# Kernel tuning notes

Measured on AMD Instinct MI355X. Metric: run time of the kernel, lower is better.

## Reference

```python
import jax, jax.numpy as jnp
import numpy as np

FILTER_P = 0.5
LOG_CLAMP = -100.0  # torch BCELoss clamps log terms at -100


def _zs_substep(img, step):
    """One Zhang-Suen thinning sub-iteration. img: int32 [H, W] in {0,1}.
    skimage.morphology.skeletonize uses Zhang-Suen for 2D inputs."""
    p = jnp.pad(img, 1)
    P2 = p[:-2, 1:-1]; P3 = p[:-2, 2:];  P4 = p[1:-1, 2:];  P5 = p[2:, 2:]
    P6 = p[2:, 1:-1];  P7 = p[2:, :-2];  P8 = p[1:-1, :-2]; P9 = p[:-2, :-2]
    nbrs = jnp.stack([P2, P3, P4, P5, P6, P7, P8, P9, P2])  # cyclic order
    B = nbrs[:8].sum(0)                                      # neighbor count
    A = ((nbrs[:-1] == 0) & (nbrs[1:] == 1)).sum(0)          # 0->1 transitions
    if step == 0:
        c1 = P2 * P4 * P6 == 0
        c2 = P4 * P6 * P8 == 0
    else:
        c1 = P2 * P4 * P8 == 0
        c2 = P2 * P6 * P8 == 0
    remove = (img == 1) & (B >= 2) & (B <= 6) & (A == 1) & c1 & c2
    return img * (1 - remove.astype(img.dtype))


def skeletonize(mask):
    """Zhang-Suen skeletonization. mask: bool [H, W] -> bool [H, W]."""
    img0 = mask.astype(jnp.int32)

    def body(state):
        img, _ = state
        new = _zs_substep(_zs_substep(img, 0), 1)
        return new, jnp.any(new != img)

    img, _ = jax.lax.while_loop(lambda s: s[1], body, (img0, jnp.bool_(True)))
    return img == 1


def setup_inputs() -> dict:
    key = jax.random.key(0)
    k1, k2 = jax.random.split(key)
    B, C, H, W = 8, 1, 512, 512
    pred = jax.random.uniform(k1, (B, C, H, W), dtype=jnp.float32)
    target = jax.random.uniform(k2, (B, C, H, W), dtype=jnp.float32)
    return {"pred": pred, "target": target}


def reference(pred, target):
    # [B, 1, H, W] -> [B, H, W]  (matches pred[i].squeeze(0))
    p2 = pred[:, 0]
    t2 = target[:, 0].astype(pred.dtype)

    gt_bin = t2 > 0.5
    pr_bin = p2 > FILTER_P
    gt_sk = jax.vmap(skeletonize)(gt_bin)
    pr_sk = jax.vmap(skeletonize)(pr_bin)

    # xor(and(gt_sk, pred_bin), gt_sk) == gt_sk & ~pred_bin (and symmetrically)
    positive_sel = gt_sk & (~pr_bin)
    negative_sel = pr_sk & (~gt_bin)
    sel = jax.lax.stop_gradient(positive_sel | negative_sel)

    # BCE with torch-style log clamping, masked mean per sample
    logp = jnp.clip(jnp.log(p2), LOG_CLAMP)
    log1mp = jnp.clip(jnp.log1p(-p2), LOG_CLAMP)
    bce = -(t2 * logp + (1.0 - t2) * log1mp)

    m = sel.astype(pred.dtype)
    cnt = m.sum(axis=(1, 2))                     # [B]
    per = jnp.where(cnt > 0,
                    (bce * m).sum(axis=(1, 2)) / jnp.maximum(cnt, 1.0),
                    0.0)
    total = per.sum() / pred.shape[0]
    return jnp.reshape(total, (1,))
```

## Files before the change

### kernel.cpp

```cpp
#include <hip/hip_runtime.h>
#include <stdint.h>

#define HW 512
#define WPR 8
#define IMG_WORDS (HW * WPR)
#define NIMG 8
#define PIX_PER_IMG (HW * HW)
#define TOTAL_PIX (NIMG * PIX_PER_IMG)
#define MASK_WORDS (TOTAL_PIX / 64)

#define NTASK 16
#define NSTRIP 16
#define SROWS 32
#define GW 16
#define BROWS 64
#define RSTRIDE 9
#define CS 16
#define MAXCHUNK 38

#define CONV_U32 (NTASK * 64)
#define HALO_U64 (NTASK * 15 * 2 * 2 * 128)

#define NBCE (TOTAL_PIX / 2048)

__global__ __launch_bounds__(256) void init_kernel(uint32_t* __restrict__ conv) {
#pragma unroll
    for (int k = 0; k < 4; ++k) conv[threadIdx.x + k * 256] = 0u;
}

__device__ __forceinline__ uint64_t zs1(int step, const uint64_t (&Uw)[3],
                                        const uint64_t (&Cw)[3],
                                        const uint64_t (&Dw)[3],
                                        uint64_t& NEW) {
    uint64_t P2 = Uw[1];
    uint64_t P6 = Dw[1];
    uint64_t P4 = (Cw[1] >> 1) | (Cw[2] << 63);
    uint64_t P8 = (Cw[1] << 1) | (Cw[0] >> 63);
    uint64_t P3 = (Uw[1] >> 1) | (Uw[2] << 63);
    uint64_t P9 = (Uw[1] << 1) | (Uw[0] >> 63);
    uint64_t P5 = (Dw[1] >> 1) | (Dw[2] << 63);
    uint64_t P7 = (Dw[1] << 1) | (Dw[0] >> 63);

    uint64_t s1 = P2 ^ P3, sum1 = s1 ^ P4, car1 = (P2 & P3) | (P4 & s1);
    uint64_t s2 = P5 ^ P6, sum2 = s2 ^ P7, car2 = (P5 & P6) | (P7 & s2);
    uint64_t s3 = sum1 ^ sum2, sum3 = s3 ^ P8, car3 = (sum1 & sum2) | (P8 & s3);
    uint64_t b0 = sum3 ^ P9, car4 = sum3 & P9;
    uint64_t s5 = car1 ^ car2, sum5 = s5 ^ car3, car5 = (car1 & car2) | (car3 & s5);
    uint64_t b1 = sum5 ^ car4, car6 = sum5 & car4;
    uint64_t b2 = car5 ^ car6, b3 = car5 & car6;
    uint64_t ge2 = b1 | b2 | b3;
    uint64_t le6 = ~(b3 | (b0 & b1 & b2));
    uint64_t condB = ge2 & le6;

    uint64_t t0 = ~P2 & P3, t1 = ~P3 & P4, t2 = ~P4 & P5, t3 = ~P5 & P6;
    uint64_t t4 = ~P6 & P7, t5 = ~P7 & P8, t6 = ~P8 & P9, t7 = ~P9 & P2;
    uint64_t a01 = t0 | t1, a23 = t2 | t3, a45 = t4 | t5, a67 = t6 | t7;
    uint64_t m2 = (t0 & t1) | (t2 & t3) | (t4 & t5) | (t6 & t7);
    uint64_t a0123 = a01 | a23, a4567 = a45 | a67;
    m2 |= (a01 & a23) | (a45 & a67);
    m2 |= a0123 & a4567;
    uint64_t condA = (a0123 | a4567) & ~m2;

    uint64_t c1, c2;
    if (step == 0) {
        uint64_t q = P4 & P6;
        c1 = ~(q & P2);
        c2 = ~(q & P8);
    } else {
        uint64_t q = P2 & P8;
        c1 = ~(q & P4);
        c2 = ~(q & P6);
    }
    uint64_t rem = Cw[1] & condB & condA & c1 & c2;
    NEW = Cw[1] & ~rem;
    return rem;
}

__global__ __launch_bounds__(512) void skel_kernel(const float* __restrict__ pred,
                                                   const float* __restrict__ target,
                                                   uint64_t* __restrict__ sk,
                                                   uint64_t* __restrict__ halo,
                                                   uint32_t* __restrict__ conv) {
    __shared__ uint64_t sbuf[2][BROWS * RSTRIDE];
    __shared__ int s_any8[8];
    __shared__ int s_dec;
    const int tid = threadIdx.x;
    const int task = blockIdx.x & (NTASK - 1);
    const int strip = blockIdx.x >> 4;
    const int rl = tid >> 3;
    const int wq = tid & 7;
    const int lane = tid & 63;
    const int wave = tid >> 6;
    const int gr0 = strip * SROWS - GW;
    const float* srcf = (task < 8 ? target : pred) + (size_t)(task & 7) * PIX_PER_IMG;
    uint64_t* dst = sk + (size_t)task * IMG_WORDS;

    for (int m = 0; m < 64; ++m) {
        int k = wave * 64 + m;
        int r = k >> 3, w = k & 7;
        int gr = gr0 + r;
        float f = (gr >= 0 && gr < HW) ? srcf[gr * HW + w * 64 + lane] : 0.0f;
        uint64_t bits = __ballot(f > 0.5f);
        if (lane == 0) sbuf[0][r * RSTRIDE + w] = bits;
    }
    __syncthreads();
    uint64_t C = sbuf[0][rl * RSTRIDE + wq];

    int cb = 0;
    const bool owned = (rl >= GW) && (rl < GW + SROWS);
    for (int chunk = 0; chunk < MAXCHUNK; ++chunk) {
        uint32_t tailch = 0;
        for (int ss = 0; ss < CS; ++ss) {
            const uint64_t* cur = sbuf[cb];
            uint64_t* nxt = sbuf[cb ^ 1];
            uint64_t Uw[3], Cw[3], Dw[3], NEW;
#pragma unroll
            for (int j = 0; j < 3; ++j) {
                int gw = wq - 1 + j;
                bool v = (gw >= 0) && (gw < 8);
                Uw[j] = (v && rl > 0)          ? cur[(rl - 1) * RSTRIDE + gw] : 0ull;
                Dw[j] = (v && rl < BROWS - 1)  ? cur[(rl + 1) * RSTRIDE + gw] : 0ull;
            }
            Cw[0] = (wq > 0) ? cur[rl * RSTRIDE + wq - 1] : 0ull;
            Cw[2] = (wq < 7) ? cur[rl * RSTRIDE + wq + 1] : 0ull;
            Cw[1] = C;
            uint64_t ch = zs1(ss & 1, Uw, Cw, Dw, NEW);
            if (ss >= CS - 2 && owned && ch) tailch = 1;
            nxt[rl * RSTRIDE + wq] = NEW;
            C = NEW;
            cb ^= 1;
            __syncthreads();
        }

        const int par = chunk & 1;
        if (strip > 0 && rl >= GW && rl < 2 * GW) {
            uint64_t* hp = halo + ((((size_t)task * 15 + (strip - 1)) * 2 + 0) * 2 + par) * 128
                                + (rl - GW) * 8 + wq;
            __hip_atomic_store(hp, C, __ATOMIC_RELAXED, __HIP_MEMORY_SCOPE_AGENT);
            asm volatile("s_waitcnt vmcnt(0)" ::: "memory");
        }
        if (strip < NSTRIP - 1 && rl >= 32 && rl < 48) {
            uint64_t* hp = halo + ((((size_t)task * 15 + strip) * 2 + 1) * 2 + par) * 128
                                + (rl - 32) * 8 + wq;
            __hip_atomic_store(hp, C, __ATOMIC_RELAXED, __HIP_MEMORY_SCOPE_AGENT);
            asm volatile("s_waitcnt vmcnt(0)" ::: "memory");
        }
        int wa = __any((int)tailch);
        if (lane == 0) s_any8[wave] = wa;
        __syncthreads();
        if (tid == 0) {
            int any = s_any8[0] | s_any8[1] | s_any8[2] | s_any8[3]
                    | s_any8[4] | s_any8[5] | s_any8[6] | s_any8[7];
            uint32_t add = 256u + (any ? 1u : 0u);
            uint32_t* cp = &conv[task * 64 + chunk];
            uint32_t v = __hip_atomic_fetch_add(cp, add, __ATOMIC_RELEASE,
                                                __HIP_MEMORY_SCOPE_AGENT) + add;
            while ((v >> 8) < (uint32_t)NSTRIP)
                v = __hip_atomic_load(cp, __ATOMIC_ACQUIRE, __HIP_MEMORY_SCOPE_AGENT);
            s_dec = ((v & 0xffu) != 0u) ? 1 : 0;
        }
        __syncthreads();
        if (!s_dec) break;

        if (strip > 0 && rl < GW) {
            const uint64_t* hp = halo + ((((size_t)task * 15 + (strip - 1)) * 2 + 1) * 2 + par) * 128
                                      + rl * 8 + wq;
            C = __hip_atomic_load(hp, __ATOMIC_RELAXED, __HIP_MEMORY_SCOPE_AGENT);
            sbuf[cb][rl * RSTRIDE + wq] = C;
        }
        if (strip < NSTRIP - 1 && rl >= 48) {
            const uint64_t* hp = halo + ((((size_t)task * 15 + strip) * 2 + 0) * 2 + par) * 128
                                      + (rl - 48) * 8 + wq;
            C = __hip_atomic_load(hp, __ATOMIC_RELAXED, __HIP_MEMORY_SCOPE_AGENT);
            sbuf[cb][rl * RSTRIDE + wq] = C;
        }
        __syncthreads();
    }

    if (owned) {
        int gr = gr0 + rl;
        dst[gr * WPR + wq] = C;
    }
}

__global__ __launch_bounds__(256) void bce_kernel(
        const float4* __restrict__ pred4, const float4* __restrict__ tgt4,
        const uint64_t* __restrict__ gt_sk, const uint64_t* __restrict__ pr_sk,
        float* __restrict__ psum, int* __restrict__ pcnt) {
    int tg = blockIdx.x * 256 + threadIdx.x;
    int w = tg >> 3;
    int sh = (tg & 7) * 8;
    uint32_t gbits = (uint32_t)(gt_sk[w] >> sh) & 0xffu;
    uint32_t pbits = (uint32_t)(pr_sk[w] >> sh) & 0xffu;
    float4 pa = pred4[2 * tg], pb = pred4[2 * tg + 1];
    float4 ta = tgt4[2 * tg], tb = tgt4[2 * tg + 1];
    float p[8] = {pa.x, pa.y, pa.z, pa.w, pb.x, pb.y, pb.z, pb.w};
    float t[8] = {ta.x, ta.y, ta.z, ta.w, tb.x, tb.y, tb.z, tb.w};
    float lsum = 0.0f;
    int lcnt = 0;
#pragma unroll
    for (int j = 0; j < 8; ++j) {
        float lp = fmaxf(logf(p[j]), -100.0f);
        float l1 = fmaxf(log1pf(-p[j]), -100.0f);
        float b = -(t[j] * lp + (1.0f - t[j]) * l1);
        uint32_t prb = (p[j] > 0.5f) ? 1u : 0u;
        uint32_t gtb = (t[j] > 0.5f) ? 1u : 0u;
        uint32_t m = (((gbits >> j) & 1u) & (prb ^ 1u))
                   | (((pbits >> j) & 1u) & (gtb ^ 1u));
        lsum = fmaf((float)m, b, lsum);
        lcnt += (int)m;
    }
#pragma unroll
    for (int off = 32; off > 0; off >>= 1) {
        lsum += __shfl_down(lsum, off, 64);
        lcnt += __shfl_down(lcnt, off, 64);
    }
    __shared__ float sred[4];
    __shared__ int cred[4];
    int wave = threadIdx.x >> 6, lane = threadIdx.x & 63;
    if (lane == 0) { sred[wave] = lsum; cred[wave] = lcnt; }
    __syncthreads();
    if (threadIdx.x == 0) {
        psum[blockIdx.x] = sred[0] + sred[1] + sred[2] + sred[3];
        pcnt[blockIdx.x] = cred[0] + cred[1] + cred[2] + cred[3];
    }
}

__global__ __launch_bounds__(1024) void final_kernel(const float* __restrict__ psum,
                                                     const int* __restrict__ pcnt,
                                                     float* __restrict__ out) {
    int t = threadIdx.x;
    float s = psum[t];
    int c = pcnt[t];
#pragma unroll
    for (int off = 32; off > 0; off >>= 1) {
        s += __shfl_down(s, off, 64);
        c += __shfl_down(c, off, 64);
    }
    __shared__ float ss[16];
    __shared__ int sc[16];
    int w = t >> 6;
    if ((t & 63) == 0) { ss[w] = s; sc[w] = c; }
    __syncthreads();
    if (t == 0) {
        float tot = 0.0f;
#pragma unroll
        for (int i = 0; i < NIMG; ++i) {
            float sv = ss[2 * i] + ss[2 * i + 1];
            int cv = sc[2 * i] + sc[2 * i + 1];
            tot += (cv > 0) ? sv / (float)cv : 0.0f;
        }
        out[0] = tot * (1.0f / NIMG);
    }
}

extern "C" void kernel_launch(void* const* d_in, const int* in_sizes, int n_in,
                              void* d_out, int out_size, void* d_ws, size_t ws_size,
                              hipStream_t stream) {
    const float* pred = (const float*)d_in[0];
    const float* target = (const float*)d_in[1];
    uint64_t* ws = (uint64_t*)d_ws;
    uint64_t* sk    = ws;
    uint64_t* gt_sk = sk;
    uint64_t* pr_sk = sk + MASK_WORDS;
    uint64_t* halo  = ws + 2 * MASK_WORDS;
    uint32_t* conv  = (uint32_t*)(halo + HALO_U64);
    float* psum     = (float*)(conv + CONV_U32);
    int* pcnt       = (int*)(psum + NBCE);

    init_kernel<<<1, 256, 0, stream>>>(conv);
    skel_kernel<<<NTASK * NSTRIP, 512, 0, stream>>>(pred, target, sk, halo, conv);
    bce_kernel<<<NBCE, 256, 0, stream>>>((const float4*)pred, (const float4*)target,
                                         gt_sk, pr_sk, psum, pcnt);
    final_kernel<<<1, 1024, 0, stream>>>(psum, pcnt, (float*)d_out);
}
```

Measured before the change: 111.0 us.

## Pre-pack binary masks in separate kernel and transpose skeleton LDS layout

Adds a pack_kernel that thresholds pred and target into bit masks across many blocks, and folds the convergence-counter zeroing into that kernel. The skeleton kernel now loads pre-packed 64-bit words instead of reading floats and running ballots per strip, including the redundant halo rows. Shared memory is transposed to word-column-major with stride 65, so each wave owns one word column across 64 rows. This shortens the serial prologue of the persistent skeleton blocks, at the cost of an extra launch and a global bitmask round trip.

```diff
diff --git a/kernel.cpp b/kernel.cpp
--- a/kernel.cpp
+++ b/kernel.cpp
@@ -14,7 +14,7 @@
 #define SROWS 32
 #define GW 16
 #define BROWS 64
-#define RSTRIDE 9
+#define LSTRIDE 65
 #define CS 16
 #define MAXCHUNK 38
 
@@ -23,9 +23,25 @@
 
 #define NBCE (TOTAL_PIX / 2048)
 
-__global__ __launch_bounds__(256) void init_kernel(uint32_t* __restrict__ conv) {
-#pragma unroll
-    for (int k = 0; k < 4; ++k) conv[threadIdx.x + k * 256] = 0u;
+__global__ void pack_kernel(const float* __restrict__ pred,
+                            const float* __restrict__ target,
+                            uint64_t* __restrict__ gt_bin,
+                            uint64_t* __restrict__ pr_bin,
+                            uint32_t* __restrict__ conv) {
+    int idx = blockIdx.x * 256 + threadIdx.x;
+    if (blockIdx.x < 4) {
+        int z = blockIdx.x * 256 + threadIdx.x;
+        conv[z] = 0u;
+    }
+    float p = pred[idx];
+    float t = target[idx];
+    uint64_t bp = __ballot(p > 0.5f);
+    uint64_t bt = __ballot(t > 0.5f);
+    if ((threadIdx.x & 63) == 0) {
+        int w = idx >> 6;
+        pr_bin[w] = bp;
+        gt_bin[w] = bt;
+    }
 }
 
 __device__ __forceinline__ uint64_t zs1(int step, const uint64_t (&Uw)[3],
@@ -76,35 +92,30 @@
     return rem;
 }
 
-__global__ __launch_bounds__(512) void skel_kernel(const float* __restrict__ pred,
-                                                   const float* __restrict__ target,
+__global__ __launch_bounds__(512) void skel_kernel(const uint64_t* __restrict__ bin,
                                                    uint64_t* __restrict__ sk,
                                                    uint64_t* __restrict__ halo,
                                                    uint32_t* __restrict__ conv) {
-    __shared__ uint64_t sbuf[2][BROWS * RSTRIDE];
+    __shared__ uint64_t sbuf[2][WPR * LSTRIDE];
     __shared__ int s_any8[8];
     __shared__ int s_dec;
     const int tid = threadIdx.x;
     const int task = blockIdx.x & (NTASK - 1);
     const int strip = blockIdx.x >> 4;
-    const int rl = tid >> 3;
-    const int wq = tid & 7;
-    const int lane = tid & 63;
-    const int wave = tid >> 6;
+    const int wq = tid >> 6;
+    const int rl = tid & 63;
     const int gr0 = strip * SROWS - GW;
-    const float* srcf = (task < 8 ? target : pred) + (size_t)(task & 7) * PIX_PER_IMG;
+    const uint64_t* src = bin + (size_t)task * IMG_WORDS;
     uint64_t* dst = sk + (size_t)task * IMG_WORDS;
 
-    for (int m = 0; m < 64; ++m) {
-        int k = wave * 64 + m;
-        int r = k >> 3, w = k & 7;
-        int gr = gr0 + r;
-        float f = (gr >= 0 && gr < HW) ? srcf[gr * HW + w * 64 + lane] : 0.0f;
-        uint64_t bits = __ballot(f > 0.5f);
-        if (lane == 0) sbuf[0][r * RSTRIDE + w] = bits;
+    uint64_t C;
+    {
+        int gr = gr0 + rl;
+        bool in = (gr >= 0) && (gr < HW);
+        C = in ? src[gr * WPR + wq] : 0ull;
+        sbuf[0][wq * LSTRIDE + rl] = C;
     }
     __syncthreads();
-    uint64_t C = sbuf[0][rl * RSTRIDE + wq];
 
     int cb = 0;
     const bool owned = (rl >= GW) && (rl < GW + SROWS);
@@ -118,15 +129,15 @@
             for (int j = 0; j < 3; ++j) {
                 int gw = wq - 1 + j;
                 bool v = (gw >= 0) && (gw < 8);
-                Uw[j] = (v && rl > 0)          ? cur[(rl - 1) * RSTRIDE + gw] : 0ull;
-                Dw[j] = (v && rl < BROWS - 1)  ? cur[(rl + 1) * RSTRIDE + gw] : 0ull;
+                Uw[j] = (v && rl > 0)          ? cur[gw * LSTRIDE + rl - 1] : 0ull;
+                Dw[j] = (v && rl < BROWS - 1)  ? cur[gw * LSTRIDE + rl + 1] : 0ull;
             }
-            Cw[0] = (wq > 0) ? cur[rl * RSTRIDE + wq - 1] : 0ull;
-            Cw[2] = (wq < 7) ? cur[rl * RSTRIDE + wq + 1] : 0ull;
+            Cw[0] = (wq > 0) ? cur[(wq - 1) * LSTRIDE + rl] : 0ull;
+            Cw[2] = (wq < 7) ? cur[(wq + 1) * LSTRIDE + rl] : 0ull;
             Cw[1] = C;
             uint64_t ch = zs1(ss & 1, Uw, Cw, Dw, NEW);
             if (ss >= CS - 2 && owned && ch) tailch = 1;
-            nxt[rl * RSTRIDE + wq] = NEW;
+            nxt[wq * LSTRIDE + rl] = NEW;
             C = NEW;
             cb ^= 1;
             __syncthreads();
@@ -146,7 +157,7 @@
             asm volatile("s_waitcnt vmcnt(0)" ::: "memory");
         }
         int wa = __any((int)tailch);
-        if (lane == 0) s_any8[wave] = wa;
+        if (rl == 0) s_any8[wq] = wa;
         __syncthreads();
         if (tid == 0) {
             int any = s_any8[0] | s_any8[1] | s_any8[2] | s_any8[3]
@@ -166,13 +177,13 @@
             const uint64_t* hp = halo + ((((size_t)task * 15 + (strip - 1)) * 2 + 1) * 2 + par) * 128
                                       + rl * 8 + wq;
             C = __hip_atomic_load(hp, __ATOMIC_RELAXED, __HIP_MEMORY_SCOPE_AGENT);
-            sbuf[cb][rl * RSTRIDE + wq] = C;
+            sbuf[cb][wq * LSTRIDE + rl] = C;
         }
         if (strip < NSTRIP - 1 && rl >= 48) {
             const uint64_t* hp = halo + ((((size_t)task * 15 + strip) * 2 + 0) * 2 + par) * 128
                                       + (rl - 48) * 8 + wq;
             C = __hip_atomic_load(hp, __ATOMIC_RELAXED, __HIP_MEMORY_SCOPE_AGENT);
-            sbuf[cb][rl * RSTRIDE + wq] = C;
+            sbuf[cb][wq * LSTRIDE + rl] = C;
         }
         __syncthreads();
     }
@@ -260,16 +271,17 @@
     const float* pred = (const float*)d_in[0];
     const float* target = (const float*)d_in[1];
     uint64_t* ws = (uint64_t*)d_ws;
-    uint64_t* sk    = ws;
-    uint64_t* gt_sk = sk;
-    uint64_t* pr_sk = sk + MASK_WORDS;
-    uint64_t* halo  = ws + 2 * MASK_WORDS;
-    uint32_t* conv  = (uint32_t*)(halo + HALO_U64);
-    float* psum     = (float*)(conv + CONV_U32);
-    int* pcnt       = (int*)(psum + NBCE);
-
-    init_kernel<<<1, 256, 0, stream>>>(conv);
-    skel_kernel<<<NTASK * NSTRIP, 512, 0, stream>>>(pred, target, sk, halo, conv);
+    uint64_t* gt_bin = ws;
+    uint64_t* pr_bin = ws + MASK_WORDS;
+    uint64_t* gt_sk  = ws + 2 * MASK_WORDS;
+    uint64_t* pr_sk  = ws + 3 * MASK_WORDS;
+    uint64_t* halo   = ws + 4 * MASK_WORDS;
+    uint32_t* conv   = (uint32_t*)(halo + HALO_U64);
+    float* psum      = (float*)(conv + CONV_U32);
+    int* pcnt        = (int*)(psum + NBCE);
+
+    pack_kernel<<<TOTAL_PIX / 256, 256, 0, stream>>>(pred, target, gt_bin, pr_bin, conv);
+    skel_kernel<<<NTASK * NSTRIP, 512, 0, stream>>>(gt_bin, gt_sk, halo, conv);
     bce_kernel<<<NBCE, 256, 0, stream>>>((const float4*)pred, (const float4*)target,
                                          gt_sk, pr_sk, psum, pcnt);
     final_kernel<<<1, 1024, 0, stream>>>(psum, pcnt, (float*)d_out);
```

Result: faster. 96.68 us (-12.9%).
